# Kernel optimization log

Hardware: AMD Instinct MI355X
Metric: run time of the kernel (lower is better)

The kernel has to match this reference:

```python
import jax, jax.numpy as jnp
from jax import lax
import numpy as np

VOCAB = 128
EMB = 128
UNITS = [1024, 1024]
B, T = 64, 512


def setup_inputs() -> dict:
    key = jax.random.key(0)
    ks = jax.random.split(key, 16)
    s = 0.02
    inp = {
        "tokens": jax.random.randint(ks[0], (B, T), 0, VOCAB),
        "emb": jax.random.normal(ks[1], (VOCAB, EMB), jnp.float32) * s,
    }
    in_dims = [EMB] + UNITS[:-1]
    for i, (d_in, h) in enumerate(zip(in_dims, UNITS)):
        inp[f"W{i}"] = jax.random.normal(ks[2 + 3 * i], (d_in, 4 * h), jnp.float32) * s
        inp[f"U{i}"] = jax.random.normal(ks[3 + 3 * i], (h, 4 * h), jnp.float32) * s
        # Keras default: forget-gate bias initialized to 1 (unit_forget_bias)
        b = np.zeros((4 * h,), np.float32)
        b[h:2 * h] = 1.0
        inp[f"b{i}"] = jnp.asarray(b)
    inp["Wd"] = jax.random.normal(ks[10], (UNITS[-1], VOCAB), jnp.float32) * s
    inp["bd"] = jnp.zeros((VOCAB,), jnp.float32)
    return inp


def lstm_layer(x, W, U, b):
    # x: [B, T, D_in] -> [B, T, H]; keras gate order i, f, g(c), o
    Bm, Tm, _ = x.shape
    H = U.shape[0]
    xz = jnp.einsum('btd,dk->btk', x, W) + b  # precompute input GEMM, [B,T,4H]

    def step(carry, xz_t):
        h, c = carry
        z = xz_t + h @ U
        i, f, g, o = jnp.split(z, 4, axis=-1)
        c = jax.nn.sigmoid(f) * c + jax.nn.sigmoid(i) * jnp.tanh(g)
        h = jax.nn.sigmoid(o) * jnp.tanh(c)
        return (h, c), h

    h0 = jnp.zeros((Bm, H), x.dtype)
    (_, _), hs = lax.scan(step, (h0, h0), jnp.swapaxes(xz, 0, 1))
    return jnp.swapaxes(hs, 0, 1)  # [B, T, H]


def reference(tokens, emb, W0, U0, b0, W1, U1, b1, Wd, bd):
    x = emb[tokens]  # [B, T, EMB]
    x = lstm_layer(x, W0, U0, b0)
    x = lstm_layer(x, W1, U1, b1)
    return x @ Wd + bd  # logits [B, T, VOCAB]
```

## Files before the change

### kernel.cpp

```cpp
#include <hip/hip_runtime.h>
#include <hip/hip_cooperative_groups.h>

namespace cg = cooperative_groups;

typedef _Float16 f16;
typedef __attribute__((ext_vector_type(8))) _Float16 f16x8;
typedef __attribute__((ext_vector_type(4))) float f32x4;

#define NWG      256
#define NTHREADS 768
#define BB       64
#define TT       512
#define HH       1024
#define HD4      4096
#define VOCABB   128
#define EMBD     128

#define OFF_U0   0
#define OFF_W1U1 32768
#define OFF_TW0  98304
#define OFF_Z0   106560
#define OFF_Z1A  114752
#define OFF_Z1B  122944
#define OFF_WDC  98304
#define SMEM_BYTES 131072

#define BARR_ELEMS (34 * 64)

__device__ __forceinline__ float sigf(float x) { return 1.f / (1.f + __expf(-x)); }

__device__ __forceinline__ int swz(int base, int row, int rowstride, int k) {
    return base + row * rowstride + ((2 * k) ^ ((row & 7) << 4));
}

__device__ __forceinline__ f16x8 ld16sc(const f16* p) {
    f16x8 r;
    asm volatile("global_load_dwordx4 %0, %1, off sc0 sc1"
                 : "=v"(r) : "v"(p) : "memory");
    return r;
}

__device__ __forceinline__ void st2sc(f16* p, float v) {
    f16 h = (f16)v;
    unsigned short u;
    __builtin_memcpy(&u, &h, 2);
    asm volatile("global_store_short %0, %1, off sc0 sc1"
                 :: "v"(p), "v"(u) : "memory");
}

__device__ __forceinline__ void spin_until(unsigned* p, unsigned epoch) {
    while (__hip_atomic_load(p, __ATOMIC_RELAXED, __HIP_MEMORY_SCOPE_AGENT) < epoch)
        __builtin_amdgcn_s_sleep(1);
}

__device__ __forceinline__ void gridbar(unsigned* barr, int g, int tid, unsigned epoch) {
    asm volatile("s_waitcnt vmcnt(0)" ::: "memory");
    __syncthreads();
    if (tid == 0) {
        const int gi = g >> 4;
        unsigned* gcnt  = barr + (size_t)gi * 64;
        unsigned* gflag = barr + (size_t)(16 + gi) * 64;
        unsigned* rcnt  = barr + (size_t)32 * 64;
        unsigned old = __hip_atomic_fetch_add(gcnt, 1u, __ATOMIC_RELAXED, __HIP_MEMORY_SCOPE_AGENT);
        if (old == 16u * epoch - 1u) {
            unsigned rold = __hip_atomic_fetch_add(rcnt, 1u, __ATOMIC_RELAXED, __HIP_MEMORY_SCOPE_AGENT);
            if (rold == 16u * epoch - 1u) {
                #pragma unroll
                for (int gg = 0; gg < 16; ++gg)
                    __hip_atomic_store(barr + (size_t)(16 + gg) * 64, epoch,
                                       __ATOMIC_RELAXED, __HIP_MEMORY_SCOPE_AGENT);
            }
        }
        spin_until(gflag, epoch);
    }
    __syncthreads();
}

__global__ __launch_bounds__(NTHREADS, 3)
void lstm_fused(const int* __restrict__ tokens, const float* __restrict__ emb,
                const float* __restrict__ W0, const float* __restrict__ U0,
                const float* __restrict__ b0, const float* __restrict__ W1,
                const float* __restrict__ U1, const float* __restrict__ b1,
                const float* __restrict__ Wd, const float* __restrict__ bd,
                f16* __restrict__ wsh, float* __restrict__ out)
{
    extern __shared__ char smem[];
    cg::grid_group grid = cg::this_grid();
    const int g    = blockIdx.x;
    const int tid  = threadIdx.x;
    const int lane = tid & 63;
    const int wave = tid >> 6;

    f16* h1seq = wsh;
    f16* h0st  = wsh + (size_t)BB * TT * HH;
    f16* h1st  = h0st + 2 * BB * HH;
    unsigned* barr = (unsigned*)(h1st + 2 * BB * HH);

    {
        unsigned int* zp = (unsigned int*)h0st;
        for (int i = tid; i < 512; i += NTHREADS) zp[g * 512 + i] = 0u;
        if (g == 0)
            for (int i = tid; i < BARR_ELEMS; i += NTHREADS) barr[i] = 0u;
    }
    {
        const int c = tid & 15;
        const int orig = ((c >> 2) * HH) + 4 * g + (c & 3);
        for (int k = tid >> 4; k < HH; k += 48) {
            *(f16*)(smem + swz(OFF_U0, c, 2048, k))        = (f16)U0[(size_t)k * HD4 + orig];
            *(f16*)(smem + swz(OFF_W1U1, c, 4096, k))      = (f16)W1[(size_t)k * HD4 + orig];
            *(f16*)(smem + swz(OFF_W1U1, c, 4096, k + HH)) = (f16)U1[(size_t)k * HD4 + orig];
        }
    }
    for (int idx = tid; idx < VOCABB * 16; idx += NTHREADS) {
        int v = idx >> 4, c = idx & 15;
        int orig = ((c >> 2) * HH) + 4 * g + (c & 3);
        float acc = b0[orig];
        for (int e = 0; e < EMBD; ++e)
            acc += emb[v * EMBD + e] * W0[(size_t)e * HD4 + orig];
        ((float*)(smem + OFF_TW0))[idx] = acc;
    }
    __syncthreads();
    grid.sync();

    float c0 = 0.f, c1 = 0.f;
    const int gb = tid >> 2, gd = tid & 3;
    float* z0buf  = (float*)(smem + OFF_Z0);
    float* z1abuf = (float*)(smem + OFF_Z1A);
    float* z1bbuf = (float*)(smem + OFF_Z1B);
    float* TW0s   = (float*)(smem + OFF_TW0);

    float b1r0 = 0.f, b1r1 = 0.f, b1r2 = 0.f, b1r3 = 0.f;
    if (tid < 256) {
        b1r0 = b1[0 * HH + 4 * g + gd];
        b1r1 = b1[1 * HH + 4 * g + gd];
        b1r2 = b1[2 * HH + 4 * g + gd];
        b1r3 = b1[3 * HH + 4 * g + gd];
    }

    for (int s = 0; s <= TT; ++s) {
        const f16* h0r = h0st + (size_t)(s & 1) * BB * HH;
        const f16* h1r = h1st + (size_t)(s & 1) * BB * HH;
        const int n  = lane & 15;
        const int kq = 8 * (lane >> 4);

        if (wave < 8) {
            const int mt = wave & 3, kh = wave >> 2;
            const int arow = mt * 16 + (lane & 15);
            const f16* aptr = &h0r[(size_t)arow * HH + kh * 512 + kq];
            f16x8 av[16];
            #pragma unroll
            for (int ki = 0; ki < 16; ++ki)
                av[ki] = ld16sc(aptr + ki * 32);
            asm volatile("s_waitcnt vmcnt(0)" ::: "memory");
            __builtin_amdgcn_sched_barrier(0);
            f32x4 a0 = {0.f, 0.f, 0.f, 0.f}, a1 = {0.f, 0.f, 0.f, 0.f};
            #pragma unroll
            for (int ki = 0; ki < 16; ++ki) {
                int k = kh * 512 + ki * 32 + kq;
                f16x8 bv0 = *(const f16x8*)(smem + swz(OFF_U0, n, 2048, k));
                a0 = __builtin_amdgcn_mfma_f32_16x16x32_f16(av[ki], bv0, a0, 0, 0, 0);
                f16x8 bv1 = *(const f16x8*)(smem + swz(OFF_W1U1, n, 4096, k));
                a1 = __builtin_amdgcn_mfma_f32_16x16x32_f16(av[ki], bv1, a1, 0, 0, 0);
            }
            int r0 = mt * 16 + (lane >> 4) * 4;
            #pragma unroll
            for (int r = 0; r < 4; ++r) {
                z0buf [(kh * 64 + r0 + r) * 16 + n] = a0[r];
                z1abuf[(kh * 64 + r0 + r) * 16 + n] = a1[r];
            }
        } else {
            const int mt = wave & 3;
            const int arow = mt * 16 + (lane & 15);
            const f16* aptr = &h1r[(size_t)arow * HH + kq];
            f32x4 a1 = {0.f, 0.f, 0.f, 0.f};
            #pragma unroll
            for (int half = 0; half < 2; ++half) {
                f16x8 av[16];
                #pragma unroll
                for (int ki = 0; ki < 16; ++ki)
                    av[ki] = ld16sc(aptr + half * 512 + ki * 32);
                asm volatile("s_waitcnt vmcnt(0)" ::: "memory");
                __builtin_amdgcn_sched_barrier(0);
                #pragma unroll
                for (int ki = 0; ki < 16; ++ki) {
                    int k = half * 512 + ki * 32 + kq;
                    f16x8 bv = *(const f16x8*)(smem + swz(OFF_W1U1, n, 4096, k + HH));
                    a1 = __builtin_amdgcn_mfma_f32_16x16x32_f16(av[ki], bv, a1, 0, 0, 0);
                }
            }
            int r0 = mt * 16 + (lane >> 4) * 4;
            #pragma unroll
            for (int r = 0; r < 4; ++r) z1bbuf[(r0 + r) * 16 + n] = a1[r];
        }
        __syncthreads();

        if (tid < 256) {
            const int j = 4 * g + gd;
            if (s < TT) {
                int tok = tokens[gb * TT + s];
                float zi = z0buf[gb * 16 +  0 + gd] + z0buf[(64 + gb) * 16 +  0 + gd] + TW0s[tok * 16 +  0 + gd];
                float zf = z0buf[gb * 16 +  4 + gd] + z0buf[(64 + gb) * 16 +  4 + gd] + TW0s[tok * 16 +  4 + gd];
                float zg = z0buf[gb * 16 +  8 + gd] + z0buf[(64 + gb) * 16 +  8 + gd] + TW0s[tok * 16 +  8 + gd];
                float zo = z0buf[gb * 16 + 12 + gd] + z0buf[(64 + gb) * 16 + 12 + gd] + TW0s[tok * 16 + 12 + gd];
                c0 = sigf(zf) * c0 + sigf(zi) * tanhf(zg);
                float h0v = sigf(zo) * tanhf(c0);
                st2sc(&h0st[(size_t)((s + 1) & 1) * BB * HH + (size_t)gb * HH + j], h0v);
            }
            if (s >= 1) {
                float zi = z1abuf[gb * 16 +  0 + gd] + z1abuf[(64 + gb) * 16 +  0 + gd] + z1bbuf[gb * 16 +  0 + gd] + b1r0;
                float zf = z1abuf[gb * 16 +  4 + gd] + z1abuf[(64 + gb) * 16 +  4 + gd] + z1bbuf[gb * 16 +  4 + gd] + b1r1;
                float zg = z1abuf[gb * 16 +  8 + gd] + z1abuf[(64 + gb) * 16 +  8 + gd] + z1bbuf[gb * 16 +  8 + gd] + b1r2;
                float zo = z1abuf[gb * 16 + 12 + gd] + z1abuf[(64 + gb) * 16 + 12 + gd] + z1bbuf[gb * 16 + 12 + gd] + b1r3;
                c1 = sigf(zf) * c1 + sigf(zi) * tanhf(zg);
                float h1v = sigf(zo) * tanhf(c1);
                st2sc(&h1st[(size_t)((s + 1) & 1) * BB * HH + (size_t)gb * HH + j], h1v);
                st2sc(&h1seq[((size_t)gb * TT + (s - 1)) * HH + j], h1v);
            }
        }
        gridbar(barr, g, tid, (unsigned)(s + 1));
    }

    {
        const int r0 = g * 128;
        f32x4 accC[6];
        #pragma unroll
        for (int i = 0; i < 6; ++i) accC[i] = (f32x4){0.f, 0.f, 0.f, 0.f};

        for (int kc = 0; kc < 8; ++kc) {
            __syncthreads();
            for (int idx = tid; idx < 128 * 128; idx += NTHREADS) {
                int kk = idx >> 7, nn = idx & 127;
                *(f16*)(smem + swz(OFF_WDC, nn, 256, kk)) = (f16)Wd[(size_t)(kc * 128 + kk) * 128 + nn];
            }
            __syncthreads();
            int ti = 0;
            for (int tile = wave; tile < 64; tile += 12, ++ti) {
                int mt = tile >> 3, nt = tile & 7;
                int arow = r0 + mt * 16 + (lane & 15);
                int kq = 8 * (lane >> 4);
                int nn = nt * 16 + (lane & 15);
                f32x4 acc = accC[ti];
                #pragma unroll
                for (int k4 = 0; k4 < 4; ++k4) {
                    int k = kc * 128 + k4 * 32 + kq;
                    f16x8 av = *(const f16x8*)&h1seq[(size_t)arow * HH + k];
                    f16x8 bv = *(const f16x8*)(smem + swz(OFF_WDC, nn, 256, k4 * 32 + kq));
                    acc = __builtin_amdgcn_mfma_f32_16x16x32_f16(av, bv, acc, 0, 0, 0);
                }
                accC[ti] = acc;
            }
        }
        int ti = 0;
        for (int tile = wave; tile < 64; tile += 12, ++ti) {
            int mt = tile >> 3, nt = tile & 7;
            int row0 = r0 + mt * 16 + (lane >> 4) * 4;
            int col  = nt * 16 + (lane & 15);
            float bdv = bd[col];
            #pragma unroll
            for (int r = 0; r < 4; ++r)
                out[(size_t)(row0 + r) * 128 + col] = accC[ti][r] + bdv;
        }
    }
}

extern "C" void kernel_launch(void* const* d_in, const int* in_sizes, int n_in,
                              void* d_out, int out_size, void* d_ws, size_t ws_size,
                              hipStream_t stream) {
    const int*   tokens = (const int*)d_in[0];
    const float* emb    = (const float*)d_in[1];
    const float* W0     = (const float*)d_in[2];
    const float* U0     = (const float*)d_in[3];
    const float* b0     = (const float*)d_in[4];
    const float* W1     = (const float*)d_in[5];
    const float* U1     = (const float*)d_in[6];
    const float* b1     = (const float*)d_in[7];
    const float* Wd     = (const float*)d_in[8];
    const float* bd     = (const float*)d_in[9];
    float* out = (float*)d_out;
    f16*   ws  = (f16*)d_ws;

    (void)hipFuncSetAttribute((const void*)lstm_fused,
                              hipFuncAttributeMaxDynamicSharedMemorySize, SMEM_BYTES);

    void* args[] = { &tokens, &emb, &W0, &U0, &b0, &W1, &U1, &b1, &Wd, &bd, &ws, &out };
    (void)hipLaunchCooperativeKernel((const void*)lstm_fused, dim3(NWG), dim3(NTHREADS),
                                     args, SMEM_BYTES, stream);
}
```

Measured before the change: 6.433 ms.

## Replace atomic grid barrier with per-workgroup epoch flags and targeted waits

Drops the two-level atomic-counter grid barrier at the end of each timestep. Instead, each workgroup posts its step number to its own flag once its hidden-state stores have drained. Consumer waves poll only the flags of the workgroups whose outputs they read: the layer-0 half-K waves check 128 flags and the layer-1 waves check all 256, using one vector load per lane. This removes the serialized atomic round-trips and the central release, and lets waves start as soon as their own producers are ready, at the cost of heavier polling traffic on the flags.

```diff
diff --git a/kernel.cpp b/kernel.cpp
--- a/kernel.cpp
+++ b/kernel.cpp
@@ -6,6 +6,8 @@
 typedef _Float16 f16;
 typedef __attribute__((ext_vector_type(8))) _Float16 f16x8;
 typedef __attribute__((ext_vector_type(4))) float f32x4;
+typedef __attribute__((ext_vector_type(2))) unsigned u32x2;
+typedef __attribute__((ext_vector_type(4))) unsigned u32x4;
 
 #define NWG      256
 #define NTHREADS 768
@@ -25,7 +27,7 @@
 #define OFF_WDC  98304
 #define SMEM_BYTES 131072
 
-#define BARR_ELEMS (34 * 64)
+#define FLAG_ELEMS 256
 
 __device__ __forceinline__ float sigf(float x) { return 1.f / (1.f + __expf(-x)); }
 
@@ -48,33 +50,32 @@
                  :: "v"(p), "v"(u) : "memory");
 }
 
-__device__ __forceinline__ void spin_until(unsigned* p, unsigned epoch) {
-    while (__hip_atomic_load(p, __ATOMIC_RELAXED, __HIP_MEMORY_SCOPE_AGENT) < epoch)
+__device__ __forceinline__ void post_flag(unsigned* p, unsigned v) {
+    asm volatile("global_store_dword %0, %1, off sc0 sc1" :: "v"(p), "v"(v) : "memory");
+}
+
+__device__ __forceinline__ void wait128(const unsigned* flags, unsigned epoch, int lane) {
+    const unsigned* p = flags + 2 * lane;
+    for (;;) {
+        u32x2 v;
+        asm volatile("global_load_dwordx2 %0, %1, off sc0 sc1\n\ts_waitcnt vmcnt(0)"
+                     : "=v"(v) : "v"(p) : "memory");
+        if (__all((int)(v.x >= epoch && v.y >= epoch))) break;
         __builtin_amdgcn_s_sleep(1);
-}
-
-__device__ __forceinline__ void gridbar(unsigned* barr, int g, int tid, unsigned epoch) {
-    asm volatile("s_waitcnt vmcnt(0)" ::: "memory");
-    __syncthreads();
-    if (tid == 0) {
-        const int gi = g >> 4;
-        unsigned* gcnt  = barr + (size_t)gi * 64;
-        unsigned* gflag = barr + (size_t)(16 + gi) * 64;
-        unsigned* rcnt  = barr + (size_t)32 * 64;
-        unsigned old = __hip_atomic_fetch_add(gcnt, 1u, __ATOMIC_RELAXED, __HIP_MEMORY_SCOPE_AGENT);
-        if (old == 16u * epoch - 1u) {
-            unsigned rold = __hip_atomic_fetch_add(rcnt, 1u, __ATOMIC_RELAXED, __HIP_MEMORY_SCOPE_AGENT);
-            if (rold == 16u * epoch - 1u) {
-                #pragma unroll
-                for (int gg = 0; gg < 16; ++gg)
-                    __hip_atomic_store(barr + (size_t)(16 + gg) * 64, epoch,
-                                       __ATOMIC_RELAXED, __HIP_MEMORY_SCOPE_AGENT);
-            }
-        }
-        spin_until(gflag, epoch);
-    }
-    __syncthreads();
-}
+    }
+}
+
+__device__ __forceinline__ void wait256(const unsigned* flags, unsigned epoch, int lane) {
+    const unsigned* p = flags + 4 * lane;
+    for (;;) {
+        u32x4 v;
+        asm volatile("global_load_dwordx4 %0, %1, off sc0 sc1\n\ts_waitcnt vmcnt(0)"
+                     : "=v"(v) : "v"(p) : "memory");
+        if (__all((int)(v.x >= epoch && v.y >= epoch && v.z >= epoch && v.w >= epoch))) break;
+        __builtin_amdgcn_s_sleep(1);
+    }
+}
+
 
 __global__ __launch_bounds__(NTHREADS, 3)
 void lstm_fused(const int* __restrict__ tokens, const float* __restrict__ emb,
@@ -94,13 +95,13 @@
     f16* h1seq = wsh;
     f16* h0st  = wsh + (size_t)BB * TT * HH;
     f16* h1st  = h0st + 2 * BB * HH;
-    unsigned* barr = (unsigned*)(h1st + 2 * BB * HH);
+    unsigned* wflag = (unsigned*)(h1st + 2 * BB * HH);
 
     {
         unsigned int* zp = (unsigned int*)h0st;
         for (int i = tid; i < 512; i += NTHREADS) zp[g * 512 + i] = 0u;
         if (g == 0)
-            for (int i = tid; i < BARR_ELEMS; i += NTHREADS) barr[i] = 0u;
+            for (int i = tid; i < FLAG_ELEMS; i += NTHREADS) wflag[i] = 0u;
     }
     {
         const int c = tid & 15;
@@ -145,6 +146,7 @@
 
         if (wave < 8) {
             const int mt = wave & 3, kh = wave >> 2;
+            wait128(wflag + kh * 128, (unsigned)s, lane);
             const int arow = mt * 16 + (lane & 15);
             const f16* aptr = &h0r[(size_t)arow * HH + kh * 512 + kq];
             f16x8 av[16];
@@ -169,6 +171,7 @@
                 z1abuf[(kh * 64 + r0 + r) * 16 + n] = a1[r];
             }
         } else {
+            wait256(wflag, (unsigned)s, lane);
             const int mt = wave & 3;
             const int arow = mt * 16 + (lane & 15);
             const f16* aptr = &h1r[(size_t)arow * HH + kq];
@@ -194,7 +197,7 @@
         }
         __syncthreads();
 
-        if (tid < 256) {
+        if (wave < 4) {
             const int j = 4 * g + gd;
             if (s < TT) {
                 int tok = tokens[gb * TT + s];
@@ -216,9 +219,13 @@
                 st2sc(&h1st[(size_t)((s + 1) & 1) * BB * HH + (size_t)gb * HH + j], h1v);
                 st2sc(&h1seq[((size_t)gb * TT + (s - 1)) * HH + j], h1v);
             }
-        }
-        gridbar(barr, g, tid, (unsigned)(s + 1));
-    }
+            asm volatile("s_waitcnt vmcnt(0)" ::: "memory");
+        }
+        __syncthreads();
+        if (tid == 0) post_flag(&wflag[g], (unsigned)(s + 1));
+    }
+
+    wait256(wflag, (unsigned)(TT + 1), lane);
 
     {
         const int r0 = g * 128;
```

New measurement: 7.741 ms. +20.3%, slower.
